# Kernel tuning notes

Hardware: AMD Instinct MI355X
Metric: run time of the kernel (lower is better)

Reference implementation:

```python
import jax, jax.numpy as jnp
import numpy as np

D = 768; H = 12; DH = 64; P = 16; G = 14; NP = 196; L = 197
LD = 4; GD = 12          # local / latent depths
RL = 12; RG = 8          # tokens merged per layer (total_merge // depth)
B = 8
EPS = 1e-6


def layernorm(x, g, b):
    mu = x.mean(-1, keepdims=True)
    v = ((x - mu) ** 2).mean(-1, keepdims=True)
    return (x - mu) / jnp.sqrt(v + EPS) * g + b


def attention(x, size, qkv_w, qkv_b, pw, pb):
    # proportional attention: logits += log(token size)
    Bn, N, _ = x.shape
    qkv = (x @ qkv_w + qkv_b).reshape(Bn, N, 3, H, DH)
    q, k, v = (qkv[:, :, i].transpose(0, 2, 1, 3) for i in range(3))  # bhnd
    logits = jnp.einsum('bhqd,bhkd->bhqk', q, k) * (DH ** -0.5)
    logits = logits + jnp.log(size)[:, None, None, :, 0]
    a = jax.nn.softmax(logits, axis=-1)
    o = jnp.einsum('bhqk,bhkd->bhqd', a, v).transpose(0, 2, 1, 3).reshape(Bn, N, D)
    return o @ pw + pb, k.mean(1)  # metric = mean key over heads


def tome_merge(x, size, metric, r, tok_map):
    # ToMe bipartite soft matching + weighted-average merge + source-map update
    Bn, N, _ = x.shape
    t1, t2 = (N + 1) // 2, N // 2
    m = metric / jnp.linalg.norm(metric, axis=-1, keepdims=True)
    scores = jnp.einsum('bid,bjd->bij', m[:, ::2], m[:, 1::2])
    scores = scores.at[:, 0, :].set(-jnp.inf)  # protect cls token
    node_max, node_idx = scores.max(-1), scores.argmax(-1).astype(jnp.int32)
    order = jnp.argsort(-node_max, axis=-1).astype(jnp.int32)
    src_idx = order[:, :r]
    unm_idx = jnp.sort(order[:, r:], axis=-1)  # cls stays first
    dst_idx = jnp.take_along_axis(node_idx, src_idx, axis=1)
    bi = jnp.arange(Bn)[:, None]

    def merge_sum(v):
        a, b = v[:, ::2], v[:, 1::2]
        unm = jnp.take_along_axis(a, unm_idx[..., None], axis=1)
        s = jnp.take_along_axis(a, src_idx[..., None], axis=1)
        b = b.at[bi, dst_idx].add(s)
        return jnp.concatenate([unm, b], axis=1)

    new_size = merge_sum(size)
    new_x = merge_sum(x * size) / new_size
    # per-step old->new index map, then compose with running source map
    pos_a = jnp.zeros((Bn, t1), jnp.int32)
    pos_a = pos_a.at[bi, unm_idx].set(jnp.arange(t1 - r, dtype=jnp.int32))
    pos_a = pos_a.at[bi, src_idx].set((t1 - r) + dst_idx)
    step = jnp.zeros((Bn, N), jnp.int32)
    step = step.at[:, ::2].set(pos_a)
    step = step.at[:, 1::2].set((t1 - r) + jnp.arange(t2, dtype=jnp.int32)[None])
    return new_x, new_size, jnp.take_along_axis(step, tok_map, axis=1)


def encode(x, size, tok_map, r, p):
    ln1g, ln1b, qw, qb, pw, pb, ln2g, ln2b, f1w, f1b, f2w, f2b = p
    for i in range(ln1g.shape[0]):
        a, metric = attention(layernorm(x, ln1g[i], ln1b[i]), size, qw[i], qb[i], pw[i], pb[i])
        x = x + a
        if r > 0:
            x, size, tok_map = tome_merge(x, size, metric, r, tok_map)
        h = layernorm(x, ln2g[i], ln2b[i])
        x = x + (jax.nn.gelu(h @ f1w[i] + f1b[i], approximate=False) @ f2w[i] + f2b[i])
    return x, size, tok_map


def setup_inputs() -> dict:
    key = jax.random.key(0)
    ks = iter(jax.random.split(key, 64))
    def w(shape):
        return jax.random.normal(next(ks), shape, jnp.float32) * 0.02
    def blocks(d, pre):
        return {pre + 'ln1g': jnp.ones((d, D)), pre + 'ln1b': jnp.zeros((d, D)),
                pre + 'qkv_w': w((d, D, 3 * D)), pre + 'qkv_b': jnp.zeros((d, 3 * D)),
                pre + 'proj_w': w((d, D, D)), pre + 'proj_b': jnp.zeros((d, D)),
                pre + 'ln2g': jnp.ones((d, D)), pre + 'ln2b': jnp.zeros((d, D)),
                pre + 'fc1w': w((d, D, 4 * D)), pre + 'fc1b': jnp.zeros((d, 4 * D)),
                pre + 'fc2w': w((d, 4 * D, D)), pre + 'fc2b': jnp.zeros((d, D))}
    inp = dict(x=jax.random.normal(next(ks), (B, 3, 224, 224), jnp.float32),
               patch_w=w((3 * P * P, D)), patch_b=jnp.zeros((D,)),
               cls_tok=w((1, 1, D)), pos_emb=w((1, L, D)),
               l_ng=jnp.ones((D,)), l_nb=jnp.zeros((D,)),
               g_ng=jnp.ones((D,)), g_nb=jnp.zeros((D,)),
               head_w=w((D, 10)), head_b=jnp.zeros((10,)))
    inp.update(blocks(LD, 'l_'))
    inp.update(blocks(GD, 'g_'))
    return inp


def reference(x, patch_w, patch_b, cls_tok, pos_emb,
              l_ln1g, l_ln1b, l_qkv_w, l_qkv_b, l_proj_w, l_proj_b,
              l_ln2g, l_ln2b, l_fc1w, l_fc1b, l_fc2w, l_fc2b, l_ng, l_nb,
              g_ln1g, g_ln1b, g_qkv_w, g_qkv_b, g_proj_w, g_proj_b,
              g_ln2g, g_ln2b, g_fc1w, g_fc1b, g_fc2w, g_fc2b, g_ng, g_nb,
              head_w, head_b):
    Bn = x.shape[0]
    # non-overlapping 16x16 patchify == conv stride 16
    patches = x.reshape(Bn, 3, G, P, G, P).transpose(0, 2, 4, 1, 3, 5).reshape(Bn, NP, 3 * P * P)
    t = patches @ patch_w + patch_b
    t = jnp.concatenate([jnp.broadcast_to(cls_tok, (Bn, 1, D)), t], axis=1) + pos_emb
    size = jnp.ones((Bn, L, 1), t.dtype)
    tmap = jnp.broadcast_to(jnp.arange(L, dtype=jnp.int32)[None], (Bn, L))  # token_map_for_dtem
    lp = (l_ln1g, l_ln1b, l_qkv_w, l_qkv_b, l_proj_w, l_proj_b, l_ln2g, l_ln2b, l_fc1w, l_fc1b, l_fc2w, l_fc2b)
    xl, size, tmap = encode(t, size, tmap, RL, lp)   # local encoder: 197 -> 149 tokens
    xl = layernorm(xl, l_ng, l_nb)
    N1 = xl.shape[1]
    smap = jnp.broadcast_to(jnp.arange(N1, dtype=jnp.int32)[None], (Bn, N1))  # latent source_map
    gp = (g_ln1g, g_ln1b, g_qkv_w, g_qkv_b, g_proj_w, g_proj_b, g_ln2g, g_ln2b, g_fc1w, g_fc1b, g_fc2w, g_fc2b)
    xg, size, smap = encode(xl, size, smap, RG, gp)  # latent encoder: 149 -> 53 tokens
    xg = layernorm(xg, g_ng, g_nb)
    xr = jnp.take_along_axis(xg, smap[..., None], axis=1)   # token_unmerge_from_map (ToMe)
    xf = jnp.take_along_axis(xr, tmap[..., None], axis=1)   # token_unmerge_from_map_for_dtem
    return xf[:, 0] @ head_w + head_b  # cls token -> logits (B, 10)
```

## Files before the change

kernel.cpp:

```cpp
#include <hip/hip_runtime.h>
#include <math.h>

#define NB 8
#define SD 768
#define NHEAD 12
#define LMAX 197
#define QBLK 32
#define KBLK 64

typedef __attribute__((ext_vector_type(8))) short bf16x8;
typedef __attribute__((ext_vector_type(4))) float f32x4;
typedef const __attribute__((address_space(1))) unsigned int gu32_t;
typedef __attribute__((address_space(3))) unsigned int lu32_t;

static __device__ __forceinline__ float geluf(float x){
    return 0.5f*x*(1.0f+erff(x*0.70710678118654752440f));
}

static __device__ __forceinline__ void split_bf16(float v, ushort& h, ushort& l){
    uint u = __float_as_uint(v);
    uint hb = (u + 0x7FFFu + ((u>>16)&1u)) >> 16;
    h = (ushort)hb;
    float rem = v - __uint_as_float(hb<<16);
    uint u2 = __float_as_uint(rem);
    l = (ushort)((u2 + 0x7FFFu + ((u2>>16)&1u)) >> 16);
}

__global__ __launch_bounds__(256) void wconv(const float* __restrict__ W,
        ushort* __restrict__ Hi, ushort* __restrict__ Lo, int K, int Nc)
{
    __shared__ float tile[32][33];
    int z = blockIdx.z;
    const float* Wz = W + (size_t)z*K*Nc;
    ushort* Hz = Hi + (size_t)z*Nc*K;
    ushort* Lz = Lo + (size_t)z*Nc*K;
    int n0 = blockIdx.x*32, k0 = blockIdx.y*32;
    int tx = threadIdx.x&31, ty = threadIdx.x>>5;
    #pragma unroll
    for (int i=0;i<32;i+=8) tile[ty+i][tx] = Wz[(size_t)(k0+ty+i)*Nc + n0+tx];
    __syncthreads();
    #pragma unroll
    for (int i=0;i<32;i+=8){
        float v = tile[tx][ty+i];
        ushort h,l; split_bf16(v,h,l);
        size_t o = (size_t)(n0+ty+i)*K + k0+tx;
        Hz[o]=h; Lz[o]=l;
    }
}

template<int EPI, int SPLITK>
__global__ __launch_bounds__(256) void gemm_mfma(const ushort* __restrict__ AHi,
        const ushort* __restrict__ ALo, const ushort* __restrict__ WHi,
        const ushort* __restrict__ WLo, const float* __restrict__ bias,
        const float* __restrict__ R, float* __restrict__ C,
        ushort* __restrict__ CHi, ushort* __restrict__ CLo,
        float* __restrict__ Part, int M, int Nc, int K, int ntok, int gx)
{
    __shared__ __align__(16) ushort sAhi[2][2048], sAlo[2][2048];
    __shared__ __align__(16) ushort sBhi[2][2048], sBlo[2][2048];
    const int t = threadIdx.x;
    const int nwg = gridDim.x;
    const int qc = nwg>>3, rc = nwg&7;
    const int xcd = blockIdx.x & 7, jj = blockIdx.x >> 3;
    const int wid = (xcd<rc ? xcd*(qc+1) : rc*(qc+1)+(xcd-rc)*qc) + jj;
    const int bx = wid % gx;
    const int t2 = wid / gx;
    const int gy = nwg/(gx*SPLITK);
    const int by = t2 % gy;
    const int bz = t2 / gy;

    const int w = t>>6, l = t&63, lr = l&15, lg = l>>4;
    const int wr = w>>1, wc = w&1;

    const int Ks = K/SPLITK;
    const int kbeg = bz*Ks;
    const int nt = Ks/32;

    const int srow = t>>2;
    const uint schunk = (uint)((t&3)*16);
    int ar = by*64 + srow; if (ar >= M) ar = M-1;
    int ab_ = ar/ntok; int an_ = ar - ab_*ntok;
    size_t aoff = ((size_t)(ab_*LMAX+an_)*K + kbeg)*2 + schunk;
    size_t woff = ((size_t)(bx*64+srow)*K + kbeg)*2 + schunk;
    const char* pAh = (const char*)AHi + aoff;
    const char* pAl = (const char*)ALo + aoff;
    const char* pWh = (const char*)WHi + woff;
    const char* pWl = (const char*)WLo + woff;

    f32x4 acc[2][2];
    #pragma unroll
    for (int i=0;i<2;i++)
        #pragma unroll
        for (int j=0;j<2;j++) acc[i][j] = (f32x4){0.f,0.f,0.f,0.f};

    const uint wb = (uint)(w*512);

    auto stage = [&](int bf, int kt){
        size_t ko = (size_t)kt*64;
        __builtin_amdgcn_global_load_lds((gu32_t*)(pAh+ko), (lu32_t*)&sAhi[bf][wb], 16, 0, 0);
        __builtin_amdgcn_global_load_lds((gu32_t*)(pAl+ko), (lu32_t*)&sAlo[bf][wb], 16, 0, 0);
        __builtin_amdgcn_global_load_lds((gu32_t*)(pWh+ko), (lu32_t*)&sBhi[bf][wb], 16, 0, 0);
        __builtin_amdgcn_global_load_lds((gu32_t*)(pWl+ko), (lu32_t*)&sBlo[bf][wb], 16, 0, 0);
    };

    int buf = 0;
    stage(0, 0);
    for (int kt=0; kt<nt; ++kt){
        if (kt+1 < nt){
            stage(buf^1, kt+1);
            asm volatile("s_waitcnt vmcnt(4)" ::: "memory");
        } else {
            asm volatile("s_waitcnt vmcnt(0)" ::: "memory");
        }
        __builtin_amdgcn_s_barrier();
        bf16x8 ah[2], al[2], bh[2], bl[2];
        #pragma unroll
        for (int m=0;m<2;m++){
            uint off = (uint)((wr*32 + m*16 + lr)*64 + lg*16);
            ah[m] = *(const bf16x8*)((const char*)&sAhi[buf][0] + off);
            al[m] = *(const bf16x8*)((const char*)&sAlo[buf][0] + off);
        }
        #pragma unroll
        for (int n=0;n<2;n++){
            uint off = (uint)((wc*32 + n*16 + lr)*64 + lg*16);
            bh[n] = *(const bf16x8*)((const char*)&sBhi[buf][0] + off);
            bl[n] = *(const bf16x8*)((const char*)&sBlo[buf][0] + off);
        }
        #pragma unroll
        for (int m=0;m<2;m++)
            #pragma unroll
            for (int n=0;n<2;n++){
                acc[m][n] = __builtin_amdgcn_mfma_f32_16x16x32_bf16(ah[m], bh[n], acc[m][n], 0,0,0);
                acc[m][n] = __builtin_amdgcn_mfma_f32_16x16x32_bf16(ah[m], bl[n], acc[m][n], 0,0,0);
                acc[m][n] = __builtin_amdgcn_mfma_f32_16x16x32_bf16(al[m], bh[n], acc[m][n], 0,0,0);
            }
        __builtin_amdgcn_s_barrier();
        buf ^= 1;
    }

    if (SPLITK > 1){
        float* Pz = Part + (size_t)bz*M*Nc;
        #pragma unroll
        for (int m=0;m<2;m++){
            #pragma unroll
            for (int n=0;n<2;n++){
                int gcol = bx*64 + wc*32 + n*16 + lr;
                #pragma unroll
                for (int r=0;r<4;r++){
                    int grow = by*64 + wr*32 + m*16 + lg*4 + r;
                    if (grow >= M) continue;
                    Pz[(size_t)grow*Nc + gcol] = acc[m][n][r];
                }
            }
        }
    } else {
        #pragma unroll
        for (int m=0;m<2;m++){
            #pragma unroll
            for (int n=0;n<2;n++){
                int gcol = bx*64 + wc*32 + n*16 + lr;
                float bv = bias[gcol];
                #pragma unroll
                for (int r=0;r<4;r++){
                    int grow = by*64 + wr*32 + m*16 + lg*4 + r;
                    if (grow >= M) continue;
                    int b = grow/ntok; int ni = grow - b*ntok;
                    size_t off = (size_t)(b*LMAX+ni)*Nc + gcol;
                    float v = acc[m][n][r] + bv;
                    if (EPI==1){
                        v = geluf(v);
                        ushort h,lo; split_bf16(v,h,lo);
                        CHi[off]=h; CLo[off]=lo;
                    } else {
                        if (EPI==2) v += R[off];
                        C[off] = v;
                    }
                }
            }
        }
    }
}

__global__ __launch_bounds__(256) void reduce_k(const float* __restrict__ P,
        const float* __restrict__ bias, const float* __restrict__ R,
        float* __restrict__ C, int M, int Nc, int S, int ntok)
{
    int idx = blockIdx.x*256 + threadIdx.x;
    int tot = M*(Nc/4);
    if (idx >= tot) return;
    int grow = idx/(Nc/4), c4 = idx - grow*(Nc/4);
    size_t po = (size_t)grow*Nc + c4*4;
    float4 a = *(const float4*)(P + po);
    for (int s=1;s<S;s++){
        float4 v = *(const float4*)(P + (size_t)s*M*Nc + po);
        a.x+=v.x; a.y+=v.y; a.z+=v.z; a.w+=v.w;
    }
    int b = grow/ntok, n = grow - b*ntok;
    size_t off = (size_t)(b*LMAX+n)*Nc + c4*4;
    float4 bv = *(const float4*)(bias + c4*4);
    float4 rv = *(const float4*)(R + off);
    float4 o;
    o.x=a.x+bv.x+rv.x; o.y=a.y+bv.y+rv.y; o.z=a.z+bv.z+rv.z; o.w=a.w+bv.w+rv.w;
    *(float4*)(C + off) = o;
}

__device__ __forceinline__ float block_sum256(float v){
    __shared__ float red[4];
    for (int o=32;o>0;o>>=1) v += __shfl_down(v,o,64);
    int t=threadIdx.x;
    if ((t&63)==0) red[t>>6]=v;
    __syncthreads();
    float r = red[0]+red[1]+red[2]+red[3];
    __syncthreads();
    return r;
}

__global__ __launch_bounds__(256) void ln_split(const float* __restrict__ X,
        const float* __restrict__ gam, const float* __restrict__ bet,
        ushort* __restrict__ YHi, ushort* __restrict__ YLo)
{
    int n = blockIdx.x, b = blockIdx.y, t = threadIdx.x;
    const float* xr = X + ((size_t)(b*LMAX+n))*SD;
    size_t ro = ((size_t)(b*LMAX+n))*SD;
    float v0=xr[t], v1=xr[t+256], v2=xr[t+512];
    float mu = block_sum256(v0+v1+v2) * (1.0f/768.0f);
    float d0=v0-mu, d1=v1-mu, d2=v2-mu;
    float var = block_sum256(d0*d0+d1*d1+d2*d2) * (1.0f/768.0f);
    float rs = rsqrtf(var + 1e-6f);
    float y0 = d0*rs*gam[t]     + bet[t];
    float y1 = d1*rs*gam[t+256] + bet[t+256];
    float y2 = d2*rs*gam[t+512] + bet[t+512];
    ushort h,lo;
    split_bf16(y0,h,lo); YHi[ro+t]=h;     YLo[ro+t]=lo;
    split_bf16(y1,h,lo); YHi[ro+t+256]=h; YLo[ro+t+256]=lo;
    split_bf16(y2,h,lo); YHi[ro+t+512]=h; YLo[ro+t+512]=lo;
}

__global__ __launch_bounds__(256) void ln_kernel(const float* __restrict__ X,
        const float* __restrict__ gam, const float* __restrict__ bet,
        float* __restrict__ Y)
{
    int n = blockIdx.x, b = blockIdx.y, t = threadIdx.x;
    const float* xr = X + ((size_t)(b*LMAX+n))*SD;
    float* yr = Y + ((size_t)(b*LMAX+n))*SD;
    float v0=xr[t], v1=xr[t+256], v2=xr[t+512];
    float mu = block_sum256(v0+v1+v2) * (1.0f/768.0f);
    float d0=v0-mu, d1=v1-mu, d2=v2-mu;
    float var = block_sum256(d0*d0+d1*d1+d2*d2) * (1.0f/768.0f);
    float rs = rsqrtf(var + 1e-6f);
    yr[t]     = d0*rs*gam[t]     + bet[t];
    yr[t+256] = d1*rs*gam[t+256] + bet[t+256];
    yr[t+512] = d2*rs*gam[t+512] + bet[t+512];
}

__global__ __launch_bounds__(256) void attn_tile(const float* __restrict__ QKV,
        const float* __restrict__ SZ, ushort* __restrict__ OHi,
        ushort* __restrict__ OLo, int N)
{
    const int q0 = blockIdx.x*QBLK;
    const int h = blockIdx.y, b = blockIdx.z, t = threadIdx.x;
    __shared__ float Qs[QBLK][68];
    __shared__ float KVs[KBLK][68];
    __shared__ float Ls[QBLK][200];
    __shared__ float szl[KBLK];
    __shared__ float invs[QBLK];

    {
        int row = t>>3, seg = t&7;
        int q = q0 + row;
        if (q < N){
            const float* src = QKV + ((size_t)(b*LMAX+q))*2304 + h*64 + seg*8;
            *(float4*)&Qs[row][seg*8]   = *(const float4*)src;
            *(float4*)&Qs[row][seg*8+4] = *(const float4*)(src+4);
        } else {
            float4 z = make_float4(0.f,0.f,0.f,0.f);
            *(float4*)&Qs[row][seg*8]   = z;
            *(float4*)&Qs[row][seg*8+4] = z;
        }
    }
    const int tq = t>>3, tk = t&7;
    const int nkt = (N+KBLK-1)/KBLK;

    for (int kt=0; kt<nkt; ++kt){
        int kbase = kt*KBLK;
        __syncthreads();
        {
            int row = t>>2, seg = t&3;
            int ktok = kbase + row;
            float4 a,b4,c,d4;
            if (ktok < N){
                const float* src = QKV + ((size_t)(b*LMAX+ktok))*2304 + 768 + h*64 + seg*16;
                a=*(const float4*)src; b4=*(const float4*)(src+4);
                c=*(const float4*)(src+8); d4=*(const float4*)(src+12);
            } else {
                a=b4=c=d4=make_float4(0.f,0.f,0.f,0.f);
            }
            *(float4*)&KVs[row][seg*16]   =a;
            *(float4*)&KVs[row][seg*16+4] =b4;
            *(float4*)&KVs[row][seg*16+8] =c;
            *(float4*)&KVs[row][seg*16+12]=d4;
            if (t < KBLK){
                int kk2 = kbase + t;
                szl[t] = (kk2<N) ? logf(SZ[b*LMAX+kk2]) : 0.f;
            }
        }
        __syncthreads();
        float acc[8];
        #pragma unroll
        for (int j=0;j<8;j++) acc[j]=0.f;
        #pragma unroll 4
        for (int d4=0; d4<16; ++d4){
            float4 qv = *(const float4*)&Qs[tq][d4*4];
            #pragma unroll
            for (int j=0;j<8;j++){
                float4 kv = *(const float4*)&KVs[tk+8*j][d4*4];
                acc[j] += qv.x*kv.x + qv.y*kv.y + qv.z*kv.z + qv.w*kv.w;
            }
        }
        #pragma unroll
        for (int j=0;j<8;j++){
            int kk = kbase + tk + 8*j;
            if (kk < N) Ls[tq][kk] = acc[j]*0.125f + szl[tk+8*j];
        }
    }
    __syncthreads();

    {
        float m = -INFINITY;
        for (int k=tk;k<N;k+=8) m = fmaxf(m, Ls[tq][k]);
        #pragma unroll
        for (int o=1;o<8;o<<=1) m = fmaxf(m, __shfl_xor(m,o,64));
        float s = 0.f;
        for (int k=tk;k<N;k+=8){
            float p = expf(Ls[tq][k]-m);
            Ls[tq][k]=p; s+=p;
        }
        #pragma unroll
        for (int o=1;o<8;o<<=1) s += __shfl_xor(s,o,64);
        if (tk==0) invs[tq] = 1.0f/s;
    }

    float o0[8];
    #pragma unroll
    for (int i=0;i<8;i++) o0[i]=0.f;
    for (int kt=0; kt<nkt; ++kt){
        int kbase = kt*KBLK;
        __syncthreads();
        {
            int row = t>>2, seg = t&3;
            int ktok = kbase + row;
            float4 a,b4,c,d4;
            if (ktok < N){
                const float* src = QKV + ((size_t)(b*LMAX+ktok))*2304 + 1536 + h*64 + seg*16;
                a=*(const float4*)src; b4=*(const float4*)(src+4);
                c=*(const float4*)(src+8); d4=*(const float4*)(src+12);
            } else {
                a=b4=c=d4=make_float4(0.f,0.f,0.f,0.f);
            }
            *(float4*)&KVs[row][seg*16]   =a;
            *(float4*)&KVs[row][seg*16+4] =b4;
            *(float4*)&KVs[row][seg*16+8] =c;
            *(float4*)&KVs[row][seg*16+12]=d4;
        }
        __syncthreads();
        int kmax = N - kbase; if (kmax > KBLK) kmax = KBLK;
        for (int kk=0; kk<kmax; ++kk){
            float p = Ls[tq][kbase+kk];
            float4 v0 = *(const float4*)&KVs[kk][tk*8];
            float4 v1 = *(const float4*)&KVs[kk][tk*8+4];
            o0[0]+=p*v0.x; o0[1]+=p*v0.y; o0[2]+=p*v0.z; o0[3]+=p*v0.w;
            o0[4]+=p*v1.x; o0[5]+=p*v1.y; o0[6]+=p*v1.z; o0[7]+=p*v1.w;
        }
    }
    int q = q0 + tq;
    if (q < N){
        float inv = invs[tq];
        ushort hh[8], ll[8];
        #pragma unroll
        for (int i=0;i<8;i++){ split_bf16(o0[i]*inv, hh[i], ll[i]); }
        size_t o = ((size_t)(b*LMAX+q))*SD + h*64 + tk*8;
        *(ushort4*)(OHi+o)   = make_ushort4(hh[0],hh[1],hh[2],hh[3]);
        *(ushort4*)(OHi+o+4) = make_ushort4(hh[4],hh[5],hh[6],hh[7]);
        *(ushort4*)(OLo+o)   = make_ushort4(ll[0],ll[1],ll[2],ll[3]);
        *(ushort4*)(OLo+o+4) = make_ushort4(ll[4],ll[5],ll[6],ll[7]);
    }
}

__global__ void metric_k(const float* __restrict__ QKV, float* __restrict__ MET)
{
    const int n = blockIdx.x, b = blockIdx.y, d = threadIdx.x;
    const float* base = QKV + ((size_t)(b*LMAX+n))*2304 + 768 + d;
    float s=0.f;
    #pragma unroll
    for (int h=0;h<12;h++) s += base[h*64];
    s *= (1.0f/12.0f);
    float sq = s*s;
    for (int o=32;o>0;o>>=1) sq += __shfl_down(sq,o,64);
    float nrm = sqrtf(__shfl(sq,0,64));
    MET[((size_t)(b*LMAX+n))*64 + d] = s/nrm;
}

__global__ __launch_bounds__(128) void scores_k(const float* __restrict__ MET,
        float* __restrict__ NMAX, int* __restrict__ NIDX, int t2)
{
    const int i = blockIdx.x, b = blockIdx.y, t = threadIdx.x;
    __shared__ float ma[64];
    __shared__ float vals[128];
    __shared__ int idxs[128];
    if (t<64) ma[t] = MET[((size_t)(b*LMAX+2*i))*64+t];
    __syncthreads();
    float val = -INFINITY;
    if (t<t2 && i>0){
        const float* mb = MET + ((size_t)(b*LMAX+2*t+1))*64;
        float dot=0.f;
        #pragma unroll 8
        for (int dd=0;dd<64;dd++) dot += ma[dd]*mb[dd];
        val = dot;
    }
    vals[t]=val; idxs[t]=t; __syncthreads();
    for (int s=64;s>0;s>>=1){
        if (t<s){
            float v2=vals[t+s], v1=vals[t]; int i2=idxs[t+s];
            if (v2>v1 || (v2==v1 && i2<idxs[t])){ vals[t]=v2; idxs[t]=i2; }
        }
        __syncthreads();
    }
    if (t==0){ NMAX[b*128+i]=vals[0]; NIDX[b*128+i]=idxs[0]; }
}

__global__ __launch_bounds__(128) void plan_k(const float* __restrict__ NMAX,
        const int* __restrict__ NIDX, int* __restrict__ SRC, int* __restrict__ DST,
        int* __restrict__ STEP, int* __restrict__ INV, int t1, int t2, int r)
{
    const int b = blockIdx.x, i = threadIdx.x;
    __shared__ float nm[128];
    __shared__ int issrc[128];
    nm[i] = (i<t1) ? NMAX[b*128+i] : INFINITY;
    __syncthreads();
    int rank=0, is=0, ni=0;
    if (i<t1){
        float m = nm[i];
        for (int j=0;j<t1;j++){ float a=nm[j]; if (a>m || (a==m && j<i)) rank++; }
        is = (rank<r) ? 1:0;
        ni = NIDX[b*128+i];
    }
    issrc[i]=is; __syncthreads();
    if (i<t1){
        if (is){ SRC[b*16+rank]=i; DST[b*16+rank]=ni; STEP[b*LMAX+2*i] = t1-r+ni; }
        else {
            int cnt=0;
            for (int j=0;j<i;j++) cnt += 1-issrc[j];
            STEP[b*LMAX+2*i]=cnt;
            INV[b*LMAX+cnt]=2*i;
        }
    }
    if (i<t2){ STEP[b*LMAX+2*i+1]=t1-r+i; INV[b*LMAX+(t1-r)+i]=2*i+1; }
}

__global__ __launch_bounds__(256) void merge_fused(const float* __restrict__ X,
        const float* __restrict__ SZ, const int* __restrict__ INV,
        const int* __restrict__ SRC, const int* __restrict__ DST,
        float* __restrict__ XO, float* __restrict__ SZO, int t1, int r)
{
    int p = blockIdx.x, b = blockIdx.y, t = threadIdx.x;
    int base = t1 - r;
    float acc0, acc1, acc2, snew;
    if (p < base){
        int tok = INV[b*LMAX+p];
        float s = SZ[b*LMAX+tok];
        const float* xr = X + (size_t)(b*LMAX+tok)*SD;
        acc0=xr[t]*s; acc1=xr[t+256]*s; acc2=xr[t+512]*s; snew=s;
    } else {
        int d = p - base;
        int tok = 2*d+1;
        float s = SZ[b*LMAX+tok];
        const float* xr = X + (size_t)(b*LMAX+tok)*SD;
        acc0=xr[t]*s; acc1=xr[t+256]*s; acc2=xr[t+512]*s; snew=s;
        for (int k=0;k<r;k++){
            if (DST[b*16+k]==d){
                int st = 2*SRC[b*16+k];
                float ss = SZ[b*LMAX+st];
                const float* xs = X + (size_t)(b*LMAX+st)*SD;
                acc0+=xs[t]*ss; acc1+=xs[t+256]*ss; acc2+=xs[t+512]*ss; snew+=ss;
            }
        }
    }
    float inv = 1.0f/snew;
    float* o = XO + (size_t)(b*LMAX+p)*SD;
    o[t]=acc0*inv; o[t+256]=acc1*inv; o[t+512]=acc2*inv;
    if (t==0) SZO[b*LMAX+p]=snew;
}

__global__ void map_upd(int* __restrict__ MAP, const int* __restrict__ STEP, int mlen)
{
    int i = blockIdx.x*256+threadIdx.x;
    if (i >= NB*mlen) return;
    int b=i/mlen, t=i-b*mlen;
    MAP[b*LMAX+t] = STEP[b*LMAX + MAP[b*LMAX+t]];
}

__global__ void patchify(const float* __restrict__ X, ushort* __restrict__ PHi,
        ushort* __restrict__ PLo)
{
    size_t i = (size_t)blockIdx.x*256 + threadIdx.x;
    if (i >= (size_t)NB*196*768) return;
    int f = i % 768; size_t q = i/768; int p = q % 196; int b = q/196;
    int c = f >> 8, py = (f>>4)&15, px = f&15;
    int gy = p/14, gx = p - gy*14;
    float v = X[(((size_t)b*3 + c)*224 + gy*16+py)*224 + gx*16+px];
    ushort h,l; split_bf16(v,h,l);
    size_t o = ((size_t)(b*LMAX+p))*768 + f;
    PHi[o]=h; PLo[o]=l;
}

__global__ void assemble(const float* __restrict__ T, const float* __restrict__ cls,
        const float* __restrict__ pos, float* __restrict__ Xo)
{
    size_t i = (size_t)blockIdx.x*256 + threadIdx.x;
    if (i >= (size_t)NB*LMAX*768) return;
    int d = i % 768; size_t q = i/768; int n = q % LMAX; int b = q/LMAX;
    float v = (n==0) ? cls[d] : T[((size_t)(b*LMAX+n-1))*768+d];
    Xo[((size_t)(b*LMAX+n))*768+d] = v + pos[n*768+d];
}

__global__ void init_state(float* __restrict__ SZ, int* __restrict__ TMAP, int* __restrict__ SMAP)
{
    int i = blockIdx.x*256+threadIdx.x;
    if (i >= NB*LMAX) return;
    SZ[i]=1.0f;
    int n=i%LMAX;
    TMAP[i]=n;
    if (n<149) SMAP[i]=n;
}

__global__ void head_k(const float* __restrict__ XG, const int* __restrict__ SMAP,
        const int* __restrict__ TMAP, const float* __restrict__ HW,
        const float* __restrict__ HB, float* __restrict__ OUT)
{
    int t = threadIdx.x;
    if (t>=80) return;
    int b=t/10, o=t-b*10;
    int row = SMAP[b*LMAX + TMAP[b*LMAX]];
    const float* xr = XG + ((size_t)(b*LMAX+row))*SD;
    float acc = HB[o];
    for (int d=0;d<SD;d++) acc += xr[d]*HW[d*10+o];
    OUT[b*10+o]=acc;
}

extern "C" void kernel_launch(void* const* d_in, const int* in_sizes, int n_in,
                              void* d_out, int out_size, void* d_ws, size_t ws_size,
                              hipStream_t stream)
{
    const float* x_in    = (const float*)d_in[0];
    const float* patch_w = (const float*)d_in[1];
    const float* patch_b = (const float*)d_in[2];
    const float* cls     = (const float*)d_in[3];
    const float* pos     = (const float*)d_in[4];
    const float* l_ng    = (const float*)d_in[5];
    const float* l_nb    = (const float*)d_in[6];
    const float* g_ng    = (const float*)d_in[7];
    const float* g_nb    = (const float*)d_in[8];
    const float* head_w  = (const float*)d_in[9];
    const float* head_b  = (const float*)d_in[10];
    const float* L[12];  for (int i=0;i<12;i++) L[i]  = (const float*)d_in[11+i];
    const float* Gp[12]; for (int i=0;i<12;i++) Gp[i] = (const float*)d_in[23+i];
    float* out = (float*)d_out;

    float* fp = (float*)d_ws;
    float* xA      = fp; fp += (size_t)NB*LMAX*SD;
    float* xB      = fp; fp += (size_t)NB*LMAX*SD;
    float* qkvbuf  = fp; fp += (size_t)NB*LMAX*2304;
    float* metricbuf=fp; fp += (size_t)NB*LMAX*64;
    float* partbuf = fp; fp += (size_t)4*NB*LMAX*SD;
    float* szA     = fp; fp += NB*LMAX;
    float* szB     = fp; fp += NB*LMAX;
    float* nodemax = fp; fp += NB*128;
    int* ip = (int*)fp;
    int* tmap    = ip; ip += NB*LMAX;
    int* smap    = ip; ip += NB*LMAX;
    int* stepbuf = ip; ip += NB*LMAX;
    int* invrow  = ip; ip += NB*LMAX;
    int* nodeidx = ip; ip += NB*128;
    int* srcs    = ip; ip += NB*16;
    int* dsts    = ip; ip += NB*16;
    uintptr_t up = ((uintptr_t)ip + 15) & ~(uintptr_t)15;
    ushort* sp = (ushort*)up;
    ushort* lnHi = sp; sp += (size_t)NB*LMAX*SD;
    ushort* lnLo = sp; sp += (size_t)NB*LMAX*SD;
    ushort* oHi  = sp; sp += (size_t)NB*LMAX*SD;
    ushort* oLo  = sp; sp += (size_t)NB*LMAX*SD;
    ushort* hHi  = sp; sp += (size_t)NB*LMAX*3072;
    ushort* hLo  = sp; sp += (size_t)NB*LMAX*3072;
    ushort* pHi  = sp; sp += (size_t)NB*LMAX*SD;
    ushort* pLo  = sp; sp += (size_t)NB*LMAX*SD;
    ushort* patchHi = sp; sp += (size_t)768*768;
    ushort* patchLo = sp; sp += (size_t)768*768;
    ushort* qkvHi = sp; sp += (size_t)4*768*2304;
    ushort* qkvLo = sp; sp += (size_t)4*768*2304;
    ushort* projHi= sp; sp += (size_t)4*768*768;
    ushort* projLo= sp; sp += (size_t)4*768*768;
    ushort* fc1Hi = sp; sp += (size_t)4*768*3072;
    ushort* fc1Lo = sp; sp += (size_t)4*768*3072;
    ushort* fc2Hi = sp; sp += (size_t)4*3072*768;
    ushort* fc2Lo = sp; sp += (size_t)4*3072*768;

    float *xc = xA, *xn = xB, *szc = szA, *szn = szB;

    auto conv_chunk = [&](const float* qw, const float* pw, const float* f1w,
                          const float* f2w, int nz)
    {
        wconv<<<dim3(2304/32,768/32,nz),256,0,stream>>>(qw, qkvHi, qkvLo, SD, 2304);
        wconv<<<dim3(768/32,768/32,nz),256,0,stream>>>(pw, projHi, projLo, SD, SD);
        wconv<<<dim3(3072/32,768/32,nz),256,0,stream>>>(f1w, fc1Hi, fc1Lo, SD, 3072);
        wconv<<<dim3(768/32,3072/32,nz),256,0,stream>>>(f2w, fc2Hi, fc2Lo, 3072, SD);
    };

    auto run_block = [&](const float* ln1g, const float* ln1b, const float* qb,
                         const float* pb, const float* ln2g, const float* ln2b,
                         const float* f1b, const float* f2b,
                         int slot, int N, int r, int* mp, int mlen)
    {
        int M = NB*N;
        int Mt = (M+63)/64;
        const ushort* qH = qkvHi + (size_t)slot*768*2304;
        const ushort* qL = qkvLo + (size_t)slot*768*2304;
        const ushort* pH = projHi + (size_t)slot*768*768;
        const ushort* pL = projLo + (size_t)slot*768*768;
        const ushort* f1H = fc1Hi + (size_t)slot*768*3072;
        const ushort* f1L = fc1Lo + (size_t)slot*768*3072;
        const ushort* f2H = fc2Hi + (size_t)slot*3072*768;
        const ushort* f2L = fc2Lo + (size_t)slot*3072*768;

        ln_split<<<dim3(N,NB),256,0,stream>>>(xc, ln1g, ln1b, lnHi, lnLo);
        gemm_mfma<0,1><<<36*Mt,256,0,stream>>>(lnHi, lnLo, qH, qL, qb, nullptr, qkvbuf, nullptr, nullptr, nullptr, M, 2304, SD, N, 36);
        attn_tile<<<dim3((N+QBLK-1)/QBLK,NHEAD,NB),256,0,stream>>>(qkvbuf, szc, oHi, oLo, N);
        metric_k<<<dim3(N,NB),64,0,stream>>>(qkvbuf, metricbuf);
        gemm_mfma<0,4><<<12*Mt*4,256,0,stream>>>(oHi, oLo, pH, pL, nullptr, nullptr, nullptr, nullptr, nullptr, partbuf, M, SD, SD, N, 12);
        reduce_k<<<(M*(SD/4)+255)/256,256,0,stream>>>(partbuf, pb, xc, xc, M, SD, 4, N);
        int t1=(N+1)/2, t2=N/2, Nn=N-r;
        scores_k<<<dim3(t1,NB),128,0,stream>>>(metricbuf, nodemax, nodeidx, t2);
        plan_k<<<NB,128,0,stream>>>(nodemax, nodeidx, srcs, dsts, stepbuf, invrow, t1, t2, r);
        merge_fused<<<dim3(Nn,NB),256,0,stream>>>(xc, szc, invrow, srcs, dsts, xn, szn, t1, r);
        map_upd<<<(NB*mlen+255)/256,256,0,stream>>>(mp, stepbuf, mlen);
        int M2 = NB*Nn;
        int M2t = (M2+63)/64;
        ln_split<<<dim3(Nn,NB),256,0,stream>>>(xn, ln2g, ln2b, lnHi, lnLo);
        gemm_mfma<1,1><<<48*M2t,256,0,stream>>>(lnHi, lnLo, f1H, f1L, f1b, nullptr, nullptr, hHi, hLo, nullptr, M2, 3072, SD, Nn, 48);
        gemm_mfma<0,4><<<12*M2t*4,256,0,stream>>>(hHi, hLo, f2H, f2L, nullptr, nullptr, nullptr, nullptr, nullptr, partbuf, M2, SD, 3072, Nn, 12);
        reduce_k<<<(M2*(SD/4)+255)/256,256,0,stream>>>(partbuf, f2b, xn, xn, M2, SD, 4, Nn);
        float* tf; tf=xc; xc=xn; xn=tf; tf=szc; szc=szn; szn=tf;
    };

    {
        int tot = NB*196*768;
        patchify<<<(tot+255)/256,256,0,stream>>>(x_in, pHi, pLo);
        wconv<<<dim3(768/32,768/32,1),256,0,stream>>>(patch_w, patchHi, patchLo, SD, SD);
        gemm_mfma<0,1><<<12*((NB*196+63)/64),256,0,stream>>>(pHi, pLo, patchHi, patchLo, patch_b, nullptr, qkvbuf, nullptr, nullptr, nullptr, NB*196, SD, SD, 196, 12);
        int tot2 = NB*LMAX*768;
        assemble<<<(tot2+255)/256,256,0,stream>>>(qkvbuf, cls, pos, xc);
        init_state<<<(NB*LMAX+255)/256,256,0,stream>>>(szc, tmap, smap);
    }

    conv_chunk(L[2], L[4], L[8], L[10], 4);
    int N = 197;
    for (int i=0;i<4;i++){
        run_block(L[0]+i*768, L[1]+i*768, L[3]+(size_t)i*2304,
                  L[5]+(size_t)i*768, L[6]+i*768, L[7]+i*768,
                  L[9]+(size_t)i*3072, L[11]+(size_t)i*768,
                  i, N, 12, tmap, 197);
        N -= 12;
    }
    ln_kernel<<<dim3(N,NB),256,0,stream>>>(xc, l_ng, l_nb, xc);

    for (int c=0;c<3;c++){
        conv_chunk(Gp[2]+(size_t)(4*c)*768*2304, Gp[4]+(size_t)(4*c)*768*768,
                   Gp[8]+(size_t)(4*c)*768*3072, Gp[10]+(size_t)(4*c)*3072*768, 4);
        for (int j=0;j<4;j++){
            int i = 4*c+j;
            run_block(Gp[0]+i*768, Gp[1]+i*768, Gp[3]+(size_t)i*2304,
                      Gp[5]+(size_t)i*768, Gp[6]+i*768, Gp[7]+i*768,
                      Gp[9]+(size_t)i*3072, Gp[11]+(size_t)i*768,
                      j, N, 8, smap, 149);
            N -= 8;
        }
    }
    ln_kernel<<<dim3(N,NB),256,0,stream>>>(xc, g_ng, g_nb, qkvbuf);
    head_k<<<1,128,0,stream>>>(qkvbuf, smap, tmap, head_w, head_b, out);
}
```

Measured before the change: 2.753 ms.

## Fuse layernorm into split-K reduce and merge kernels, fold map update into planner

The split-K partial reduction is now done per row and, when a next block exists, also computes that block's LN1 and writes the bf16 hi/lo operands. LN2 is fused into the token-merge kernel, and the source-map update is folded into the planning kernel through a shared-memory step table. Together these remove the standalone ln_split and map_upd launches for most layers, along with their global round trips. The cost is one block per row with a quarter of the threads idle in the reduce, plus extra block reductions inside the merge kernel.

```diff
diff --git a/kernel.cpp b/kernel.cpp
--- a/kernel.cpp
+++ b/kernel.cpp
@@ -181,29 +181,6 @@
     }
 }
 
-__global__ __launch_bounds__(256) void reduce_k(const float* __restrict__ P,
-        const float* __restrict__ bias, const float* __restrict__ R,
-        float* __restrict__ C, int M, int Nc, int S, int ntok)
-{
-    int idx = blockIdx.x*256 + threadIdx.x;
-    int tot = M*(Nc/4);
-    if (idx >= tot) return;
-    int grow = idx/(Nc/4), c4 = idx - grow*(Nc/4);
-    size_t po = (size_t)grow*Nc + c4*4;
-    float4 a = *(const float4*)(P + po);
-    for (int s=1;s<S;s++){
-        float4 v = *(const float4*)(P + (size_t)s*M*Nc + po);
-        a.x+=v.x; a.y+=v.y; a.z+=v.z; a.w+=v.w;
-    }
-    int b = grow/ntok, n = grow - b*ntok;
-    size_t off = (size_t)(b*LMAX+n)*Nc + c4*4;
-    float4 bv = *(const float4*)(bias + c4*4);
-    float4 rv = *(const float4*)(R + off);
-    float4 o;
-    o.x=a.x+bv.x+rv.x; o.y=a.y+bv.y+rv.y; o.z=a.z+bv.z+rv.z; o.w=a.w+bv.w+rv.w;
-    *(float4*)(C + off) = o;
-}
-
 __device__ __forceinline__ float block_sum256(float v){
     __shared__ float red[4];
     for (int o=32;o>0;o>>=1) v += __shfl_down(v,o,64);
@@ -213,6 +190,52 @@
     float r = red[0]+red[1]+red[2]+red[3];
     __syncthreads();
     return r;
+}
+
+template<int HASLN>
+__global__ __launch_bounds__(256) void reduce_ln(const float* __restrict__ P,
+        const float* __restrict__ bias, const float* __restrict__ R,
+        float* __restrict__ C, const float* __restrict__ gam,
+        const float* __restrict__ bet, ushort* __restrict__ YHi,
+        ushort* __restrict__ YLo, int M, int ntok)
+{
+    int row = blockIdx.x, t = threadIdx.x;
+    int b = row/ntok, n = row - b*ntok;
+    size_t off = (size_t)(b*LMAX+n)*SD;
+    float4 x = make_float4(0.f,0.f,0.f,0.f);
+    int col = t*4;
+    if (t < 192){
+        size_t po = (size_t)row*SD + col;
+        float4 a  = *(const float4*)(P + po);
+        float4 a1 = *(const float4*)(P + (size_t)M*SD + po);
+        float4 a2 = *(const float4*)(P + (size_t)2*M*SD + po);
+        float4 a3 = *(const float4*)(P + (size_t)3*M*SD + po);
+        a.x+=a1.x; a.y+=a1.y; a.z+=a1.z; a.w+=a1.w;
+        a.x+=a2.x; a.y+=a2.y; a.z+=a2.z; a.w+=a2.w;
+        a.x+=a3.x; a.y+=a3.y; a.z+=a3.z; a.w+=a3.w;
+        float4 bv = *(const float4*)(bias + col);
+        float4 rv = *(const float4*)(R + off + col);
+        x.x=a.x+bv.x+rv.x; x.y=a.y+bv.y+rv.y; x.z=a.z+bv.z+rv.z; x.w=a.w+bv.w+rv.w;
+        *(float4*)(C + off + col) = x;
+    }
+    if (HASLN){
+        float mu = block_sum256(x.x+x.y+x.z+x.w) * (1.0f/768.0f);
+        float d0=x.x-mu, d1=x.y-mu, d2=x.z-mu, d3=x.w-mu;
+        float ss = (t<192) ? (d0*d0+d1*d1+d2*d2+d3*d3) : 0.f;
+        float var = block_sum256(ss) * (1.0f/768.0f);
+        float rs = rsqrtf(var + 1e-6f);
+        if (t < 192){
+            float4 gv = *(const float4*)(gam + col);
+            float4 bv2 = *(const float4*)(bet + col);
+            float y0=d0*rs*gv.x+bv2.x, y1=d1*rs*gv.y+bv2.y;
+            float y2=d2*rs*gv.z+bv2.z, y3=d3*rs*gv.w+bv2.w;
+            ushort h0,l0,h1,l1,h2,l2,h3,l3;
+            split_bf16(y0,h0,l0); split_bf16(y1,h1,l1);
+            split_bf16(y2,h2,l2); split_bf16(y3,h3,l3);
+            *(ushort4*)(YHi+off+col) = make_ushort4(h0,h1,h2,h3);
+            *(ushort4*)(YLo+off+col) = make_ushort4(l0,l1,l2,l3);
+        }
+    }
 }
 
 __global__ __launch_bounds__(256) void ln_split(const float* __restrict__ X,
@@ -428,13 +451,15 @@
     if (t==0){ NMAX[b*128+i]=vals[0]; NIDX[b*128+i]=idxs[0]; }
 }
 
-__global__ __launch_bounds__(128) void plan_k(const float* __restrict__ NMAX,
+__global__ __launch_bounds__(128) void plan_map(const float* __restrict__ NMAX,
         const int* __restrict__ NIDX, int* __restrict__ SRC, int* __restrict__ DST,
-        int* __restrict__ STEP, int* __restrict__ INV, int t1, int t2, int r)
+        int* __restrict__ INV, int* __restrict__ MAP,
+        int t1, int t2, int r, int mlen)
 {
     const int b = blockIdx.x, i = threadIdx.x;
     __shared__ float nm[128];
     __shared__ int issrc[128];
+    __shared__ int sstep[208];
     nm[i] = (i<t1) ? NMAX[b*128+i] : INFINITY;
     __syncthreads();
     int rank=0, is=0, ni=0;
@@ -446,21 +471,26 @@
     }
     issrc[i]=is; __syncthreads();
     if (i<t1){
-        if (is){ SRC[b*16+rank]=i; DST[b*16+rank]=ni; STEP[b*LMAX+2*i] = t1-r+ni; }
+        if (is){ SRC[b*16+rank]=i; DST[b*16+rank]=ni; sstep[2*i] = t1-r+ni; }
         else {
             int cnt=0;
             for (int j=0;j<i;j++) cnt += 1-issrc[j];
-            STEP[b*LMAX+2*i]=cnt;
+            sstep[2*i]=cnt;
             INV[b*LMAX+cnt]=2*i;
         }
     }
-    if (i<t2){ STEP[b*LMAX+2*i+1]=t1-r+i; INV[b*LMAX+(t1-r)+i]=2*i+1; }
-}
-
-__global__ __launch_bounds__(256) void merge_fused(const float* __restrict__ X,
+    if (i<t2){ sstep[2*i+1]=t1-r+i; INV[b*LMAX+(t1-r)+i]=2*i+1; }
+    __syncthreads();
+    for (int idx=i; idx<mlen; idx+=128)
+        MAP[b*LMAX+idx] = sstep[MAP[b*LMAX+idx]];
+}
+
+__global__ __launch_bounds__(256) void merge_ln(const float* __restrict__ X,
         const float* __restrict__ SZ, const int* __restrict__ INV,
         const int* __restrict__ SRC, const int* __restrict__ DST,
-        float* __restrict__ XO, float* __restrict__ SZO, int t1, int r)
+        const float* __restrict__ gam, const float* __restrict__ bet,
+        float* __restrict__ XO, float* __restrict__ SZO,
+        ushort* __restrict__ YHi, ushort* __restrict__ YLo, int t1, int r)
 {
     int p = blockIdx.x, b = blockIdx.y, t = threadIdx.x;
     int base = t1 - r;
@@ -486,17 +516,22 @@
         }
     }
     float inv = 1.0f/snew;
-    float* o = XO + (size_t)(b*LMAX+p)*SD;
-    o[t]=acc0*inv; o[t+256]=acc1*inv; o[t+512]=acc2*inv;
+    float x0=acc0*inv, x1=acc1*inv, x2=acc2*inv;
+    size_t ro = (size_t)(b*LMAX+p)*SD;
+    float* o = XO + ro;
+    o[t]=x0; o[t+256]=x1; o[t+512]=x2;
     if (t==0) SZO[b*LMAX+p]=snew;
-}
-
-__global__ void map_upd(int* __restrict__ MAP, const int* __restrict__ STEP, int mlen)
-{
-    int i = blockIdx.x*256+threadIdx.x;
-    if (i >= NB*mlen) return;
-    int b=i/mlen, t=i-b*mlen;
-    MAP[b*LMAX+t] = STEP[b*LMAX + MAP[b*LMAX+t]];
+    float mu = block_sum256(x0+x1+x2) * (1.0f/768.0f);
+    float d0=x0-mu, d1=x1-mu, d2=x2-mu;
+    float var = block_sum256(d0*d0+d1*d1+d2*d2) * (1.0f/768.0f);
+    float rs = rsqrtf(var + 1e-6f);
+    float y0 = d0*rs*gam[t]     + bet[t];
+    float y1 = d1*rs*gam[t+256] + bet[t+256];
+    float y2 = d2*rs*gam[t+512] + bet[t+512];
+    ushort h,lo;
+    split_bf16(y0,h,lo); YHi[ro+t]=h;     YLo[ro+t]=lo;
+    split_bf16(y1,h,lo); YHi[ro+t+256]=h; YLo[ro+t+256]=lo;
+    split_bf16(y2,h,lo); YHi[ro+t+512]=h; YLo[ro+t+512]=lo;
 }
 
 __global__ void patchify(const float* __restrict__ X, ushort* __restrict__ PHi,
@@ -578,7 +613,6 @@
     int* ip = (int*)fp;
     int* tmap    = ip; ip += NB*LMAX;
     int* smap    = ip; ip += NB*LMAX;
-    int* stepbuf = ip; ip += NB*LMAX;
     int* invrow  = ip; ip += NB*LMAX;
     int* nodeidx = ip; ip += NB*128;
     int* srcs    = ip; ip += NB*16;
@@ -618,7 +652,8 @@
     auto run_block = [&](const float* ln1g, const float* ln1b, const float* qb,
                          const float* pb, const float* ln2g, const float* ln2b,
                          const float* f1b, const float* f2b,
-                         int slot, int N, int r, int* mp, int mlen)
+                         int slot, int N, int r, int* mp, int mlen,
+                         bool lead, const float* nln_g, const float* nln_b)
     {
         int M = NB*N;
         int Mt = (M+63)/64;
@@ -631,23 +666,25 @@
         const ushort* f2H = fc2Hi + (size_t)slot*3072*768;
         const ushort* f2L = fc2Lo + (size_t)slot*3072*768;
 
-        ln_split<<<dim3(N,NB),256,0,stream>>>(xc, ln1g, ln1b, lnHi, lnLo);
+        if (lead)
+            ln_split<<<dim3(N,NB),256,0,stream>>>(xc, ln1g, ln1b, lnHi, lnLo);
         gemm_mfma<0,1><<<36*Mt,256,0,stream>>>(lnHi, lnLo, qH, qL, qb, nullptr, qkvbuf, nullptr, nullptr, nullptr, M, 2304, SD, N, 36);
         attn_tile<<<dim3((N+QBLK-1)/QBLK,NHEAD,NB),256,0,stream>>>(qkvbuf, szc, oHi, oLo, N);
         metric_k<<<dim3(N,NB),64,0,stream>>>(qkvbuf, metricbuf);
         gemm_mfma<0,4><<<12*Mt*4,256,0,stream>>>(oHi, oLo, pH, pL, nullptr, nullptr, nullptr, nullptr, nullptr, partbuf, M, SD, SD, N, 12);
-        reduce_k<<<(M*(SD/4)+255)/256,256,0,stream>>>(partbuf, pb, xc, xc, M, SD, 4, N);
+        reduce_ln<0><<<M,256,0,stream>>>(partbuf, pb, xc, xc, nullptr, nullptr, nullptr, nullptr, M, N);
         int t1=(N+1)/2, t2=N/2, Nn=N-r;
         scores_k<<<dim3(t1,NB),128,0,stream>>>(metricbuf, nodemax, nodeidx, t2);
-        plan_k<<<NB,128,0,stream>>>(nodemax, nodeidx, srcs, dsts, stepbuf, invrow, t1, t2, r);
-        merge_fused<<<dim3(Nn,NB),256,0,stream>>>(xc, szc, invrow, srcs, dsts, xn, szn, t1, r);
-        map_upd<<<(NB*mlen+255)/256,256,0,stream>>>(mp, stepbuf, mlen);
+        plan_map<<<NB,128,0,stream>>>(nodemax, nodeidx, srcs, dsts, invrow, mp, t1, t2, r, mlen);
+        merge_ln<<<dim3(Nn,NB),256,0,stream>>>(xc, szc, invrow, srcs, dsts, ln2g, ln2b, xn, szn, lnHi, lnLo, t1, r);
         int M2 = NB*Nn;
         int M2t = (M2+63)/64;
-        ln_split<<<dim3(Nn,NB),256,0,stream>>>(xn, ln2g, ln2b, lnHi, lnLo);
         gemm_mfma<1,1><<<48*M2t,256,0,stream>>>(lnHi, lnLo, f1H, f1L, f1b, nullptr, nullptr, hHi, hLo, nullptr, M2, 3072, SD, Nn, 48);
         gemm_mfma<0,4><<<12*M2t*4,256,0,stream>>>(hHi, hLo, f2H, f2L, nullptr, nullptr, nullptr, nullptr, nullptr, partbuf, M2, SD, 3072, Nn, 12);
-        reduce_k<<<(M2*(SD/4)+255)/256,256,0,stream>>>(partbuf, f2b, xn, xn, M2, SD, 4, Nn);
+        if (nln_g)
+            reduce_ln<1><<<M2,256,0,stream>>>(partbuf, f2b, xn, xn, nln_g, nln_b, lnHi, lnLo, M2, Nn);
+        else
+            reduce_ln<0><<<M2,256,0,stream>>>(partbuf, f2b, xn, xn, nullptr, nullptr, nullptr, nullptr, M2, Nn);
         float* tf; tf=xc; xc=xn; xn=tf; tf=szc; szc=szn; szn=tf;
     };
 
@@ -664,10 +701,12 @@
     conv_chunk(L[2], L[4], L[8], L[10], 4);
     int N = 197;
     for (int i=0;i<4;i++){
+        const float* ng = (i<3) ? L[0]+(i+1)*768 : nullptr;
+        const float* nb2 = (i<3) ? L[1]+(i+1)*768 : nullptr;
         run_block(L[0]+i*768, L[1]+i*768, L[3]+(size_t)i*2304,
                   L[5]+(size_t)i*768, L[6]+i*768, L[7]+i*768,
                   L[9]+(size_t)i*3072, L[11]+(size_t)i*768,
-                  i, N, 12, tmap, 197);
+                  i, N, 12, tmap, 197, i==0, ng, nb2);
         N -= 12;
     }
     ln_kernel<<<dim3(N,NB),256,0,stream>>>(xc, l_ng, l_nb, xc);
@@ -677,10 +716,12 @@
                    Gp[8]+(size_t)(4*c)*768*3072, Gp[10]+(size_t)(4*c)*3072*768, 4);
         for (int j=0;j<4;j++){
             int i = 4*c+j;
+            const float* ng = (i<11) ? Gp[0]+(i+1)*768 : nullptr;
+            const float* nb2 = (i<11) ? Gp[1]+(i+1)*768 : nullptr;
             run_block(Gp[0]+i*768, Gp[1]+i*768, Gp[3]+(size_t)i*2304,
                       Gp[5]+(size_t)i*768, Gp[6]+i*768, Gp[7]+i*768,
                       Gp[9]+(size_t)i*3072, Gp[11]+(size_t)i*768,
-                      j, N, 8, smap, 149);
+                      j, N, 8, smap, 149, i==0, ng, nb2);
             N -= 8;
         }
     }
```

Result: slower. 3.168 ms (+15.1%).
